# Optimization experiments

Measured on AMD Instinct MI355X. Metric: run time of the kernel, lower is better.

## Reference

```python
import jax, jax.numpy as jnp
import numpy as np

B, C = 1, 1
D = H = W = 128          # volume depth/height/width (z, y, x)
V = U = 128              # detector rows (v) / cols (u)
A = 96                   # projection angles
N_STEPS = 128            # Joseph ray-marching steps
SX = SY = SD = 1.0       # voxel size (sd, sy, sx)
SU = SV = 1.0            # detector spacing (sv, su)


def setup_inputs() -> dict:
    key = jax.random.key(0)
    # model-facing volume [B, C, X, Y, Z]
    vol = jax.random.normal(key, (B, C, W, H, D), dtype=jnp.float32)
    angles = jnp.linspace(0.0, np.pi, A, endpoint=False).astype(jnp.float32)
    return {"vol": vol, "angles": angles}


def _corner(idx, size):
    """Floor/ceil corner indices + zero-padded linear weights (align_corners=True,
    padding_mode='zeros' semantics of F.grid_sample)."""
    i0f = jnp.floor(idx)
    frac = idx - i0f
    i0 = i0f.astype(jnp.int32)
    i1 = i0 + 1
    w0 = jnp.where((i0 >= 0) & (i0 < size), 1.0 - frac, 0.0)
    w1 = jnp.where((i1 >= 0) & (i1 < size), frac, 0.0)
    return jnp.clip(i0, 0, size - 1), jnp.clip(i1, 0, size - 1), w0, w1


def reference(vol, angles):
    # [B,C,X,Y,Z] -> [B,C,D,H,W] (z,y,x ordering used internally)
    v_zyx = jnp.transpose(vol, (0, 1, 4, 3, 2))
    cos_t = jnp.cos(angles)[:, None]   # [A,1]
    sin_t = jnp.sin(angles)[:, None]   # [A,1]
    u = (jnp.arange(U, dtype=jnp.float32) - (U - 1) / 2.0) * SU   # [U]
    v = (jnp.arange(V, dtype=jnp.float32) - (V - 1) / 2.0) * SV   # [V]
    # half ray length = half in-plane diagonal
    T = 0.5 * float(np.sqrt(((W - 1) * SX) ** 2 + ((H - 1) * SY) ** 2))
    delta_t = 2.0 * T / float(N_STEPS)

    x_base = -u[None, :] * sin_t   # [A,U] ray point at t=0
    y_base = u[None, :] * cos_t    # [A,U]
    # z depends only on detector row v; constant along the ray
    z_idx = v / SD + (D - 1) / 2.0                     # [V]
    z0, z1, wz0, wz1 = _corner(z_idx, D)
    z0, z1 = z0[:, None], z1[:, None]                  # [V,1]
    wz0, wz1 = wz0[:, None], wz1[:, None]

    t_vals = -T + (jnp.arange(N_STEPS, dtype=jnp.float32) + 0.5) * delta_t

    def step(acc, t):
        x_idx = (x_base + t * cos_t) / SX + (W - 1) / 2.0   # [A,U]
        y_idx = (y_base + t * sin_t) / SY + (H - 1) / 2.0   # [A,U]
        x0, x1, wx0, wx1 = [a[:, None, :] for a in _corner(x_idx, W)]  # [A,1,U]
        y0, y1, wy0, wy1 = [a[:, None, :] for a in _corner(y_idx, H)]  # [A,1,U]
        g = lambda zi, yi, xi: v_zyx[:, :, zi, yi, xi]      # -> [B,C,A,V,U]
        s = (wz0 * (wy0 * (wx0 * g(z0, y0, x0) + wx1 * g(z0, y0, x1))
                    + wy1 * (wx0 * g(z0, y1, x0) + wx1 * g(z0, y1, x1)))
             + wz1 * (wy0 * (wx0 * g(z1, y0, x0) + wx1 * g(z1, y0, x1))
                      + wy1 * (wx0 * g(z1, y1, x0) + wx1 * g(z1, y1, x1))))
        return acc + s, None

    acc0 = jnp.zeros((B, C, A, V, U), dtype=vol.dtype)
    acc, _ = jax.lax.scan(jax.checkpoint(step), acc0, t_vals)
    sino = acc * jnp.float32(delta_t)            # [B,C,A,V,U]
    # model-facing sinogram [B,C,X=U,A,Z=V]
    return jnp.transpose(sino, (0, 1, 4, 2, 3))
```

## Files before the change

### kernel.cpp

```cpp
#include <hip/hip_runtime.h>
#include <hip/hip_fp16.h>

namespace {
constexpr int A_N = 96;
constexpr int U_N = 128;
constexpr int V_N = 128;
constexpr int W_N = 128;
constexpr int H_N = 128;
constexpr int NSTEPS = 128;
constexpr float T_HALF = 89.80256121069154f;
constexpr float DT = 1.4031650189170554f;
constexpr float INV_DT = 1.0f / DT;
constexpr int PAD = 6;
constexpr int WP = W_N + 2 * PAD;
constexpr int ROW_BYTES = WP * 256;
constexpr int RAYS_PER_BLOCK = 8;
constexpr int BLOCK_THREADS = RAYS_PER_BLOCK * 16;
constexpr int SEGS = 2;
constexpr size_t VOLP_COLS = (size_t)WP * WP;
constexpr size_t VOLP_BYTES = VOLP_COLS * 256;
constexpr size_t SINO = (size_t)U_N * A_N * V_N;
}

__device__ __forceinline__ unsigned int packh2(float a, float b) {
    return (unsigned int)__half_as_ushort(__float2half_rn(a)) |
           ((unsigned int)__half_as_ushort(__float2half_rn(b)) << 16);
}

__global__ __launch_bounds__(256) void vol_pad_f16(
    const float* __restrict__ vol, unsigned int* __restrict__ volp)
{
    const int idx = blockIdx.x * 256 + threadIdx.x;
    if (idx >= (int)(VOLP_COLS * 16)) return;
    const int zo  = idx & 15;
    const int col = idx >> 4;
    const int yp = col % WP;
    const int xp = col / WP;
    const int x = xp - PAD;
    const int y = yp - PAD;
    uint4 o = make_uint4(0u, 0u, 0u, 0u);
    if ((unsigned)x < 128u && (unsigned)y < 128u) {
        const float* src = vol + (((size_t)x * 128 + y) << 7) + zo * 8;
        const float4 f0 = *(const float4*)(src);
        const float4 f1 = *(const float4*)(src + 4);
        o.x = packh2(f0.x, f0.y);
        o.y = packh2(f0.z, f0.w);
        o.z = packh2(f1.x, f1.y);
        o.w = packh2(f1.z, f1.w);
    }
    *(uint4*)((char*)volp + (size_t)col * 256 + zo * 16) = o;
}

__device__ __forceinline__ const char* step_base(
    const char* volc, int lane16, float i_f, float cv, float sv, float xb, float yb,
    float& fx, float& fy)
{
    const float tf = fmaf(i_f + 0.5f, DT, -T_HALF);
    const float xi = fmaf(tf, cv, xb);
    const float yi = fmaf(tf, sv, yb);
    const float fx0 = floorf(xi);
    const float fy0 = floorf(yi);
    fx = xi - fx0;
    fy = yi - fy0;
    const int x0 = (int)fx0;
    const int y0 = (int)fy0;
    const int base = (((x0 + PAD) * WP + (y0 + PAD)) << 8) + lane16;
    return volc + base;
}

__device__ __forceinline__ void consume(
    const uint4& q00, const uint4& q01, const uint4& q10, const uint4& q11,
    float fx, float fy, float* accf)
{
    const float wx0 = 1.f - fx;
    const float wy0 = 1.f - fy;
    const __half2 w00 = __float2half2_rn(wx0 * wy0);
    const __half2 w01 = __float2half2_rn(wx0 * fy);
    const __half2 w10 = __float2half2_rn(fx  * wy0);
    const __half2 w11 = __float2half2_rn(fx  * fy);
    const __half2* h00 = (const __half2*)&q00;
    const __half2* h01 = (const __half2*)&q01;
    const __half2* h10 = (const __half2*)&q10;
    const __half2* h11 = (const __half2*)&q11;
#pragma unroll
    for (int j = 0; j < 4; ++j) {
        __half2 p = __hmul2(w00, h00[j]);
        p = __hfma2(w01, h01[j], p);
        p = __hfma2(w10, h10[j], p);
        p = __hfma2(w11, h11[j], p);
        const float2 f = __half22float2(p);
        accf[2 * j]     += f.x;
        accf[2 * j + 1] += f.y;
    }
}

__global__ __launch_bounds__(BLOCK_THREADS) void joseph_fwd_inc(
    const unsigned short* __restrict__ volp,
    const float* __restrict__ angles,
    float* __restrict__ dst, float scale)
{
    const int zo  = threadIdx.x & 15;
    const int r   = threadIdx.x >> 4;
    const int u_i = blockIdx.x * RAYS_PER_BLOCK + r;
    const int a   = blockIdx.y;

    const int spseg = NSTEPS / gridDim.z;
    const int i0 = blockIdx.z * spseg;
    const int i1 = i0 + spseg;

    const float ang = angles[a];
    const float cv = cosf(ang);
    const float sv = sinf(ang);
    const float up = (float)u_i - 63.5f;
    const float xb = fmaf(-up, sv, 63.5f);
    const float yb = fmaf( up, cv, 63.5f);

    float tlo = -2.f * T_HALF, thi = 2.f * T_HALF;
    if (fabsf(cv) > 1e-6f) {
        const float ta = (-1.f - xb) / cv, tb = (128.f - xb) / cv;
        tlo = fmaxf(tlo, fminf(ta, tb));
        thi = fminf(thi, fmaxf(ta, tb));
    } else if (xb <= -1.f || xb >= 128.f) { thi = tlo - 1.f; }
    if (fabsf(sv) > 1e-6f) {
        const float ta = (-1.f - yb) / sv, tb = (128.f - yb) / sv;
        tlo = fmaxf(tlo, fminf(ta, tb));
        thi = fminf(thi, fmaxf(ta, tb));
    } else if (yb <= -1.f || yb >= 128.f) { thi = tlo - 1.f; }
    const int ilo = (int)floorf(fmaf(tlo + T_HALF, INV_DT, -0.5f)) - 1;
    const int ihi = (int)ceilf (fmaf(thi + T_HALF, INV_DT, -0.5f)) + 1;
    int lo = min(max(ilo, i0), i1);
    int hi = min(max(ihi + 1, i0), i1);
    lo &= ~1;
    hi = (hi + 1) & ~1;
    if (hi > i1 + 0) hi = min(hi, ((i1 + 1) & ~1));

    const char* __restrict__ volc = (const char*)volp;
    const int lane16 = zo << 4;

    float accf[8];
#pragma unroll
    for (int k = 0; k < 8; ++k) accf[k] = 0.f;

    for (int i = lo; i < hi; i += 2) {
        float fxA, fyA, fxB, fyB;
        const char* pA = step_base(volc, lane16, (float)i,       cv, sv, xb, yb, fxA, fyA);
        const char* pB = step_base(volc, lane16, (float)(i + 1), cv, sv, xb, yb, fxB, fyB);

        const uint4 qA00 = *(const uint4*)(pA);
        const uint4 qA01 = *(const uint4*)(pA + 256);
        const uint4 qA10 = *(const uint4*)(pA + ROW_BYTES);
        const uint4 qA11 = *(const uint4*)(pA + ROW_BYTES + 256);
        const uint4 qB00 = *(const uint4*)(pB);
        const uint4 qB01 = *(const uint4*)(pB + 256);
        const uint4 qB10 = *(const uint4*)(pB + ROW_BYTES);
        const uint4 qB11 = *(const uint4*)(pB + ROW_BYTES + 256);

        consume(qA00, qA01, qA10, qA11, fxA, fyA, accf);
        consume(qB00, qB01, qB10, qB11, fxB, fyB, accf);
    }

    float* op = dst + (size_t)blockIdx.z * SINO + ((size_t)u_i * A_N + a) * V_N + 8 * zo;
    *(float4*)(op)     = make_float4(accf[0] * scale, accf[1] * scale, accf[2] * scale, accf[3] * scale);
    *(float4*)(op + 4) = make_float4(accf[4] * scale, accf[5] * scale, accf[6] * scale, accf[7] * scale);
}

__global__ __launch_bounds__(256) void reduce_segs2(
    const float4* __restrict__ p, float4* __restrict__ out)
{
    const size_t i = (size_t)blockIdx.x * 256 + threadIdx.x;
    const size_t q = SINO / 4;
    const float4 a = p[i];
    const float4 b = p[i + q];
    out[i] = make_float4((a.x + b.x) * DT, (a.y + b.y) * DT,
                         (a.z + b.z) * DT, (a.w + b.w) * DT);
}

__global__ __launch_bounds__(256) void joseph_fwd_f32(
    const float* __restrict__ vol,
    const float* __restrict__ angles,
    float* __restrict__ out)
{
    const int zo  = threadIdx.x & 15;
    const int r   = threadIdx.x >> 4;
    const int u_i = blockIdx.x * 16 + r;
    const int a   = blockIdx.y;

    const float ang = angles[a];
    const float c = cosf(ang);
    const float s = sinf(ang);
    const float u = (float)u_i - 63.5f;
    const float xb = fmaf(-u, s, 63.5f);
    const float yb = fmaf( u, c, 63.5f);

    const float* volz = vol + 8 * zo;
    float4 accA = make_float4(0.f, 0.f, 0.f, 0.f);
    float4 accB = make_float4(0.f, 0.f, 0.f, 0.f);

    for (int i = 0; i < NSTEPS; ++i) {
        const float t  = fmaf((float)i + 0.5f, DT, -T_HALF);
        const float xi = fmaf(t, c, xb);
        const float yi = fmaf(t, s, yb);
        const float fx0f = floorf(xi);
        const float fy0f = floorf(yi);
        const int x0 = (int)fx0f;
        const int y0 = (int)fy0f;
        const float fx = xi - fx0f;
        const float fy = yi - fy0f;
        const int x1 = x0 + 1;
        const int y1 = y0 + 1;
        const float wx0 = (x0 >= 0 && x0 < W_N) ? (1.f - fx) : 0.f;
        const float wx1 = (x1 >= 0 && x1 < W_N) ? fx : 0.f;
        const float wy0 = (y0 >= 0 && y0 < H_N) ? (1.f - fy) : 0.f;
        const float wy1 = (y1 >= 0 && y1 < H_N) ? fy : 0.f;
        if ((wx0 + wx1) == 0.f || (wy0 + wy1) == 0.f) continue;
        const int cx0 = min(max(x0, 0), W_N - 1);
        const int cx1 = min(max(x1, 0), W_N - 1);
        const int cy0 = min(max(y0, 0), H_N - 1);
        const int cy1 = min(max(y1, 0), H_N - 1);
        const float* p00 = volz + ((cx0 * H_N + cy0) << 7);
        const float* p01 = volz + ((cx1 * H_N + cy0) << 7);
        const float* p10 = volz + ((cx0 * H_N + cy1) << 7);
        const float* p11 = volz + ((cx1 * H_N + cy1) << 7);
        const float4 v00a = *(const float4*)(p00);
        const float4 v00b = *(const float4*)(p00 + 4);
        const float4 v01a = *(const float4*)(p01);
        const float4 v01b = *(const float4*)(p01 + 4);
        const float4 v10a = *(const float4*)(p10);
        const float4 v10b = *(const float4*)(p10 + 4);
        const float4 v11a = *(const float4*)(p11);
        const float4 v11b = *(const float4*)(p11 + 4);
        const float w00 = wx0 * wy0, w01 = wx1 * wy0, w10 = wx0 * wy1, w11 = wx1 * wy1;
        accA.x = fmaf(w00, v00a.x, fmaf(w01, v01a.x, fmaf(w10, v10a.x, fmaf(w11, v11a.x, accA.x))));
        accA.y = fmaf(w00, v00a.y, fmaf(w01, v01a.y, fmaf(w10, v10a.y, fmaf(w11, v11a.y, accA.y))));
        accA.z = fmaf(w00, v00a.z, fmaf(w01, v01a.z, fmaf(w10, v10a.z, fmaf(w11, v11a.z, accA.z))));
        accA.w = fmaf(w00, v00a.w, fmaf(w01, v01a.w, fmaf(w10, v10a.w, fmaf(w11, v11a.w, accA.w))));
        accB.x = fmaf(w00, v00b.x, fmaf(w01, v01b.x, fmaf(w10, v10b.x, fmaf(w11, v11b.x, accB.x))));
        accB.y = fmaf(w00, v00b.y, fmaf(w01, v01b.y, fmaf(w10, v10b.y, fmaf(w11, v11b.y, accB.y))));
        accB.z = fmaf(w00, v00b.z, fmaf(w01, v01b.z, fmaf(w10, v10b.z, fmaf(w11, v11b.z, accB.z))));
        accB.w = fmaf(w00, v00b.w, fmaf(w01, v01b.w, fmaf(w10, v10b.w, fmaf(w11, v11b.w, accB.w))));
    }

    float* op = out + ((size_t)u_i * A_N + a) * V_N + 8 * zo;
    *(float4*)(op)     = make_float4(accA.x * DT, accA.y * DT, accA.z * DT, accA.w * DT);
    *(float4*)(op + 4) = make_float4(accB.x * DT, accB.y * DT, accB.z * DT, accB.w * DT);
}

extern "C" void kernel_launch(void* const* d_in, const int* in_sizes, int n_in,
                              void* d_out, int out_size, void* d_ws, size_t ws_size,
                              hipStream_t stream) {
    const float* vol    = (const float*)d_in[0];
    const float* angles = (const float*)d_in[1];
    float* out          = (float*)d_out;

    const size_t need_full = VOLP_BYTES + SEGS * SINO * sizeof(float);
    const int pad_blocks = (int)((VOLP_COLS * 16 + 255) / 256);

    if (ws_size >= VOLP_BYTES) {
        unsigned int* volp = (unsigned int*)d_ws;
        hipLaunchKernelGGL(vol_pad_f16, dim3(pad_blocks), dim3(256), 0, stream, vol, volp);
        if (ws_size >= need_full) {
            float* partial = (float*)((char*)d_ws + VOLP_BYTES);
            dim3 grid(U_N / RAYS_PER_BLOCK, A_N, SEGS);
            hipLaunchKernelGGL(joseph_fwd_inc, grid, dim3(BLOCK_THREADS), 0, stream,
                               (const unsigned short*)volp, angles, partial, 1.0f);
            hipLaunchKernelGGL(reduce_segs2, dim3(SINO / 4 / 256), dim3(256), 0, stream,
                               (const float4*)partial, (float4*)out);
        } else {
            dim3 grid(U_N / RAYS_PER_BLOCK, A_N, 1);
            hipLaunchKernelGGL(joseph_fwd_inc, grid, dim3(BLOCK_THREADS), 0, stream,
                               (const unsigned short*)volp, angles, out, DT);
        }
    } else {
        dim3 grid(U_N / 16, A_N);
        hipLaunchKernelGGL(joseph_fwd_f32, grid, dim3(256), 0, stream, vol, angles, out);
    }
}
```

Before: 112.2 us.

## Split rays into four segments and accumulate two steps in half2

Result: slower. 115.8 us (+3.3%).

```diff
diff --git a/kernel.cpp b/kernel.cpp
--- a/kernel.cpp
+++ b/kernel.cpp
@@ -16,7 +16,7 @@
 constexpr int ROW_BYTES = WP * 256;
 constexpr int RAYS_PER_BLOCK = 8;
 constexpr int BLOCK_THREADS = RAYS_PER_BLOCK * 16;
-constexpr int SEGS = 2;
+constexpr int SEGS = 4;
 constexpr size_t VOLP_COLS = (size_t)WP * WP;
 constexpr size_t VOLP_BYTES = VOLP_COLS * 256;
 constexpr size_t SINO = (size_t)U_N * A_N * V_N;
@@ -68,9 +68,9 @@
     return volc + base;
 }
 
-__device__ __forceinline__ void consume(
+__device__ __forceinline__ void consume_h2(
     const uint4& q00, const uint4& q01, const uint4& q10, const uint4& q11,
-    float fx, float fy, float* accf)
+    float fx, float fy, __half2& a0, __half2& a1, __half2& a2, __half2& a3)
 {
     const float wx0 = 1.f - fx;
     const float wy0 = 1.f - fy;
@@ -82,16 +82,10 @@
     const __half2* h01 = (const __half2*)&q01;
     const __half2* h10 = (const __half2*)&q10;
     const __half2* h11 = (const __half2*)&q11;
-#pragma unroll
-    for (int j = 0; j < 4; ++j) {
-        __half2 p = __hmul2(w00, h00[j]);
-        p = __hfma2(w01, h01[j], p);
-        p = __hfma2(w10, h10[j], p);
-        p = __hfma2(w11, h11[j], p);
-        const float2 f = __half22float2(p);
-        accf[2 * j]     += f.x;
-        accf[2 * j + 1] += f.y;
-    }
+    a0 = __hfma2(w00, h00[0], __hfma2(w01, h01[0], __hfma2(w10, h10[0], __hfma2(w11, h11[0], a0))));
+    a1 = __hfma2(w00, h00[1], __hfma2(w01, h01[1], __hfma2(w10, h10[1], __hfma2(w11, h11[1], a1))));
+    a2 = __hfma2(w00, h00[2], __hfma2(w01, h01[2], __hfma2(w10, h10[2], __hfma2(w11, h11[2], a2))));
+    a3 = __hfma2(w00, h00[3], __hfma2(w01, h01[3], __hfma2(w10, h10[3], __hfma2(w11, h11[3], a3))));
 }
 
 __global__ __launch_bounds__(BLOCK_THREADS) void joseph_fwd_inc(
@@ -132,7 +126,6 @@
     int hi = min(max(ihi + 1, i0), i1);
     lo &= ~1;
     hi = (hi + 1) & ~1;
-    if (hi > i1 + 0) hi = min(hi, ((i1 + 1) & ~1));
 
     const char* __restrict__ volc = (const char*)volp;
     const int lane16 = zo << 4;
@@ -140,6 +133,7 @@
     float accf[8];
 #pragma unroll
     for (int k = 0; k < 8; ++k) accf[k] = 0.f;
+    const __half2 hz = __float2half2_rn(0.f);
 
     for (int i = lo; i < hi; i += 2) {
         float fxA, fyA, fxB, fyB;
@@ -155,8 +149,18 @@
         const uint4 qB10 = *(const uint4*)(pB + ROW_BYTES);
         const uint4 qB11 = *(const uint4*)(pB + ROW_BYTES + 256);
 
-        consume(qA00, qA01, qA10, qA11, fxA, fyA, accf);
-        consume(qB00, qB01, qB10, qB11, fxB, fyB, accf);
+        __half2 a0 = hz, a1 = hz, a2 = hz, a3 = hz;
+        consume_h2(qA00, qA01, qA10, qA11, fxA, fyA, a0, a1, a2, a3);
+        consume_h2(qB00, qB01, qB10, qB11, fxB, fyB, a0, a1, a2, a3);
+
+        const float2 f0 = __half22float2(a0);
+        const float2 f1 = __half22float2(a1);
+        const float2 f2 = __half22float2(a2);
+        const float2 f3 = __half22float2(a3);
+        accf[0] += f0.x; accf[1] += f0.y;
+        accf[2] += f1.x; accf[3] += f1.y;
+        accf[4] += f2.x; accf[5] += f2.y;
+        accf[6] += f3.x; accf[7] += f3.y;
     }
 
     float* op = dst + (size_t)blockIdx.z * SINO + ((size_t)u_i * A_N + a) * V_N + 8 * zo;
@@ -164,15 +168,19 @@
     *(float4*)(op + 4) = make_float4(accf[4] * scale, accf[5] * scale, accf[6] * scale, accf[7] * scale);
 }
 
-__global__ __launch_bounds__(256) void reduce_segs2(
+__global__ __launch_bounds__(256) void reduce_segs4(
     const float4* __restrict__ p, float4* __restrict__ out)
 {
     const size_t i = (size_t)blockIdx.x * 256 + threadIdx.x;
     const size_t q = SINO / 4;
     const float4 a = p[i];
     const float4 b = p[i + q];
-    out[i] = make_float4((a.x + b.x) * DT, (a.y + b.y) * DT,
-                         (a.z + b.z) * DT, (a.w + b.w) * DT);
+    const float4 c = p[i + 2 * q];
+    const float4 d = p[i + 3 * q];
+    out[i] = make_float4((a.x + b.x + c.x + d.x) * DT,
+                         (a.y + b.y + c.y + d.y) * DT,
+                         (a.z + b.z + c.z + d.z) * DT,
+                         (a.w + b.w + c.w + d.w) * DT);
 }
 
 __global__ __launch_bounds__(256) void joseph_fwd_f32(
@@ -263,7 +271,7 @@
             dim3 grid(U_N / RAYS_PER_BLOCK, A_N, SEGS);
             hipLaunchKernelGGL(joseph_fwd_inc, grid, dim3(BLOCK_THREADS), 0, stream,
                                (const unsigned short*)volp, angles, partial, 1.0f);
-            hipLaunchKernelGGL(reduce_segs2, dim3(SINO / 4 / 256), dim3(256), 0, stream,
+            hipLaunchKernelGGL(reduce_segs4, dim3(SINO / 4 / 256), dim3(256), 0, stream,
                                (const float4*)partial, (float4*)out);
         } else {
             dim3 grid(U_N / RAYS_PER_BLOCK, A_N, 1);
```
